# Kernel optimization log

Hardware: AMD Instinct MI355X
Metric: run time of the kernel (lower is better)

## Reference

```python
import jax, jax.numpy as jnp
import numpy as np

B, R, N, E, L = 2, 5, 1024, 3, 2
F_IN, D_DIFF = 64, 64
IN_RET, INTER, OUT_RET = 320, 256, 256
H1, H_RET, N_CLS = 128, 320, 2
GAMMA = 2.5


def _nrm(k, shape, s=0.05):
    return jax.random.normal(k, shape, jnp.float32) * s


def setup_inputs() -> dict:
    ks = jax.random.split(jax.random.key(0), 28)
    return {
        "x_batch": jax.random.normal(ks[0], (B, R, N, F_IN), jnp.float32),
        "a_batch": jax.random.uniform(ks[1], (B, R, N, N), jnp.float32),
        "T": _nrm(ks[2], (L, R, E, N, N), 0.02),
        "theta": _nrm(ks[3], (L, R, E), 0.1),
        "fc_w": _nrm(ks[4], (L, R, D_DIFF, D_DIFF)),
        "fc_b": _nrm(ks[5], (L, R, D_DIFF)),
        "conv_w": _nrm(ks[6], (L, R, R)),
        "conv_b": _nrm(ks[7], (L, R)),
        "a0": jnp.full((L,), 0.25, jnp.float32),
        "a1": jnp.full((L,), 0.25, jnp.float32),
        "qw": _nrm(ks[8], (L, INTER, IN_RET)),
        "qb": _nrm(ks[9], (L, INTER)),
        "kw": _nrm(ks[10], (L, INTER, IN_RET)),
        "kb": _nrm(ks[11], (L, INTER)),
        "vw": _nrm(ks[12], (L, INTER, IN_RET)),
        "vb": _nrm(ks[13], (L, INTER)),
        "rw": _nrm(ks[14], (L, OUT_RET, INTER)),
        "rb": _nrm(ks[15], (L, OUT_RET)),
        "a_ret": jnp.full((L,), 0.25, jnp.float32),
        "l1_w": _nrm(ks[16], (L, H1, H_RET)),
        "l1_b": _nrm(ks[17], (L, H1)),
        "l2_w": _nrm(ks[18], (L, H_RET, OUT_RET + H1)),
        "l2_b": _nrm(ks[19], (L, H_RET)),
        "mlp1_w": _nrm(ks[20], (H1, H_RET)),
        "mlp1_b": _nrm(ks[21], (H1,)),
        "mlp2_w": _nrm(ks[22], (N_CLS, H1)),
        "mlp2_b": _nrm(ks[23], (N_CLS,)),
        "a_mlp": jnp.asarray(0.25, jnp.float32),
    }


def _prelu(x, a):
    return jnp.where(x >= 0, x, a * x)


def reference(x_batch, a_batch, T, theta, fc_w, fc_b, conv_w, conv_b, a0, a1,
              qw, qb, kw, kb, vw, vb, rw, rb, a_ret,
              l1_w, l1_b, l2_w, l2_b, mlp1_w, mlp1_b, mlp2_w, mlp2_b, a_mlp):
    i = jnp.arange(N)
    # D_gamma buffer: torch code sets gamma**(-tril(ones,-1)) = 1/gamma on the strictly-lower triangle
    D_gamma = jnp.where(i[:, None] > i[None, :], 1.0 / GAMMA, 0.0).astype(x_batch.dtype)
    h = x_batch  # [B,R,N,F]
    skip = jnp.transpose(x_batch, (0, 2, 1, 3)).reshape(B, N, R * F_IN)  # layer-0 skip source [B,N,R*F]
    for l in range(L):
        # multi-relation diffusion: sum_e theta[r,e] * T[r,e] * A[b,r]
        S = jnp.einsum('re,renm->rnm', theta[l], T[l])          # [R,N,N]
        mats = S[None] * a_batch                                 # [B,R,N,N]
        feats = jnp.einsum('brnm,brmd->brnd', mats, h)           # [B,R,N,D]
        fc = jnp.einsum('brnd,rod->brno', feats, fc_w[l]) + fc_b[l][None, :, None, :]
        diff = _prelu(fc, a0[l])
        # 1x1 conv mixes the relation (channel) axis
        u = _prelu(jnp.einsum('sr,brno->bsno', conv_w[l], diff) + conv_b[l][None, :, None, None], a1[l])
        h = u
        # retention: view each [R,N,D] sample as (time_dim=N, in_dim=R*D) (raw row-major reshape)
        xr = u.reshape(B, N, IN_RET)
        q = xr @ qw[l].T + qb[l]
        k = xr @ kw[l].T + kb[l]
        v = xr @ vw[l].T + vb[l]
        scores = jnp.einsum('bti,bsi->bts', q, k)                # [B,N,N]
        ret = jnp.einsum('bts,bsi->bti', D_gamma[None] * scores, v)
        eta = _prelu(ret @ rw[l].T + rb[l], a_ret[l])            # [B,N,OUT_RET] (time_dim==N so view is identity)
        ts = skip @ l1_w[l].T + l1_b[l]                          # [B,N,H1]
        skip = jnp.concatenate([eta, ts], axis=2) @ l2_w[l].T + l2_b[l]  # [B,N,H_RET]
    out = _prelu(skip @ mlp1_w.T + mlp1_b, a_mlp)
    return out @ mlp2_w.T + mlp2_b                               # [B,N,N_CLS]
```

## Files before the change

### kernel.cpp

```cpp
#include <hip/hip_runtime.h>

#define NB 2
#define NR 5
#define NN_ 1024
#define NL 2
#define MSPLIT 4

__global__ void init_kernel(const float* __restrict__ x, float* __restrict__ skip) {
    int idx = blockIdx.x * 256 + threadIdx.x;
    int d4 = idx & 15;
    int n = (idx >> 4) & 1023;
    int br = idx >> 14;
    int b = br / NR, r = br % NR;
    float4 v = ((const float4*)x)[idx];
    *(float4*)(skip + ((size_t)b * NN_ + n) * 320 + r * 64 + d4 * 4) = v;
}

__global__ __launch_bounds__(256) void feats_kernel(
    const float* __restrict__ T, const float* __restrict__ theta,
    const float* __restrict__ a, const float* __restrict__ h,
    float* __restrict__ part, int l) {
    __shared__ float As[32][68];
    __shared__ float Ws[32][68];
    int br = blockIdx.y;
    int b = br / NR, r = br % NR;
    int n0 = blockIdx.x * 64;
    int mz = blockIdx.z;
    int tid = threadIdx.x;
    int tx = tid & 15, ty = tid >> 4;
    const float* Tb = T + (size_t)(l * NR + r) * 3145728;
    float th0 = theta[(l * NR + r) * 3 + 0];
    float th1 = theta[(l * NR + r) * 3 + 1];
    float th2 = theta[(l * NR + r) * 3 + 2];
    const float* ab = a + (size_t)(b * NR + r) * 1048576;
    const float* hb = h + (size_t)(b * NR + r) * 65536;
    int mbeg = mz * (NN_ / MSPLIT), mend = mbeg + NN_ / MSPLIT;
    int c4 = tid & 7, nrow = tid >> 3;
    int d4 = tid & 15, mrow = tid >> 4;
    float4 pT0[2], pT1[2], pT2[2], pA[2], pH[2];
    auto LOAD = [&](int k0) {
#pragma unroll
        for (int j = 0; j < 2; ++j) {
            size_t o = (size_t)(n0 + nrow + j * 32) * 1024 + k0 + c4 * 4;
            pT0[j] = *(const float4*)(Tb + o);
            pT1[j] = *(const float4*)(Tb + 1048576 + o);
            pT2[j] = *(const float4*)(Tb + 2097152 + o);
            pA[j]  = *(const float4*)(ab + o);
        }
#pragma unroll
        for (int j = 0; j < 2; ++j)
            pH[j] = *(const float4*)(hb + (size_t)(k0 + mrow + j * 16) * 64 + d4 * 4);
    };
    float acc[4][4] = {};
    LOAD(mbeg);
    for (int k0 = mbeg; k0 < mend; k0 += 32) {
        float4 w4[2];
#pragma unroll
        for (int j = 0; j < 2; ++j) {
            w4[j].x = (th0 * pT0[j].x + th1 * pT1[j].x + th2 * pT2[j].x) * pA[j].x;
            w4[j].y = (th0 * pT0[j].y + th1 * pT1[j].y + th2 * pT2[j].y) * pA[j].y;
            w4[j].z = (th0 * pT0[j].z + th1 * pT1[j].z + th2 * pT2[j].z) * pA[j].z;
            w4[j].w = (th0 * pT0[j].w + th1 * pT1[j].w + th2 * pT2[j].w) * pA[j].w;
        }
        __syncthreads();
#pragma unroll
        for (int j = 0; j < 2; ++j) {
            int n = nrow + j * 32;
            As[c4 * 4 + 0][n] = w4[j].x; As[c4 * 4 + 1][n] = w4[j].y;
            As[c4 * 4 + 2][n] = w4[j].z; As[c4 * 4 + 3][n] = w4[j].w;
        }
#pragma unroll
        for (int j = 0; j < 2; ++j)
            *(float4*)&Ws[mrow + j * 16][d4 * 4] = pH[j];
        if (k0 + 32 < mend) LOAD(k0 + 32);
        __syncthreads();
#pragma unroll
        for (int kk = 0; kk < 32; ++kk) {
            float4 ra = *(const float4*)&As[kk][ty * 4];
            float4 rw = *(const float4*)&Ws[kk][tx * 4];
            float ar[4] = {ra.x, ra.y, ra.z, ra.w};
            float wr[4] = {rw.x, rw.y, rw.z, rw.w};
#pragma unroll
            for (int i = 0; i < 4; ++i)
#pragma unroll
                for (int j = 0; j < 4; ++j) acc[i][j] += ar[i] * wr[j];
        }
    }
    float* pb = part + ((size_t)mz * 10 + br) * 65536;
#pragma unroll
    for (int i = 0; i < 4; ++i) {
        float4 o4 = make_float4(acc[i][0], acc[i][1], acc[i][2], acc[i][3]);
        *(float4*)(pb + (size_t)(n0 + ty * 4 + i) * 64 + tx * 4) = o4;
    }
}

__global__ __launch_bounds__(256) void reduce_fc_kernel(
    const float* __restrict__ part, const float* __restrict__ fc_w,
    const float* __restrict__ fc_b, const float* __restrict__ a0,
    float* __restrict__ diff, int l) {
    __shared__ float F[64][68];
    __shared__ float Wl[64][68];
    int br = blockIdx.y;
    int r = br % NR;
    int n0 = blockIdx.x * 64;
    int tid = threadIdx.x;
    int lane = tid & 63, g = tid >> 6;
#pragma unroll
    for (int j = 0; j < 4; ++j) {
        int d4 = g + j * 4;
        size_t off = (size_t)br * 65536 + (size_t)(n0 + lane) * 64 + d4 * 4;
        float4 s = *(const float4*)(part + off);
#pragma unroll
        for (int z = 1; z < MSPLIT; ++z) {
            float4 p = *(const float4*)(part + (size_t)z * 655360 + off);
            s.x += p.x; s.y += p.y; s.z += p.z; s.w += p.w;
        }
        F[d4 * 4 + 0][lane] = s.x; F[d4 * 4 + 1][lane] = s.y;
        F[d4 * 4 + 2][lane] = s.z; F[d4 * 4 + 3][lane] = s.w;
    }
    const float* w = fc_w + (size_t)(l * NR + r) * 4096;
#pragma unroll
    for (int j = 0; j < 4; ++j) {
        int d4 = g + j * 4;
        float4 wv = *(const float4*)(w + (size_t)lane * 64 + d4 * 4);
        Wl[d4 * 4 + 0][lane] = wv.x; Wl[d4 * 4 + 1][lane] = wv.y;
        Wl[d4 * 4 + 2][lane] = wv.z; Wl[d4 * 4 + 3][lane] = wv.w;
    }
    __syncthreads();
    int tx = tid & 15, ty = tid >> 4;
    float acc[4][4] = {};
#pragma unroll
    for (int kk = 0; kk < 64; ++kk) {
        float4 ra = *(const float4*)&F[kk][ty * 4];
        float4 rw = *(const float4*)&Wl[kk][tx * 4];
        float ar[4] = {ra.x, ra.y, ra.z, ra.w};
        float wr[4] = {rw.x, rw.y, rw.z, rw.w};
#pragma unroll
        for (int i = 0; i < 4; ++i)
#pragma unroll
            for (int j = 0; j < 4; ++j) acc[i][j] += ar[i] * wr[j];
    }
    float al = a0[l];
    const float* bia = fc_b + (l * NR + r) * 64;
#pragma unroll
    for (int i = 0; i < 4; ++i) {
        float4 o4;
        float* op = &o4.x;
#pragma unroll
        for (int j = 0; j < 4; ++j) {
            float v = acc[i][j] + bia[tx * 4 + j];
            op[j] = (v >= 0.f) ? v : al * v;
        }
        *(float4*)(diff + (size_t)br * 65536 + (size_t)(n0 + ty * 4 + i) * 64 + tx * 4) = o4;
    }
}

__global__ void conv_kernel(const float* __restrict__ diff,
                            const float* __restrict__ cw, const float* __restrict__ cb,
                            const float* __restrict__ a1, float* __restrict__ u, int l) {
    int idx = blockIdx.x * 256 + threadIdx.x;
    int no4 = idx & 16383;
    int bs = idx >> 14;
    int s = bs % NR, b = bs / NR;
    const float* dbase = diff + (size_t)b * NR * 65536;
    float bias = cb[l * NR + s];
    float4 acc = make_float4(bias, bias, bias, bias);
#pragma unroll
    for (int r = 0; r < NR; ++r) {
        float w = cw[(l * NR + s) * NR + r];
        float4 dv = *(const float4*)(dbase + (size_t)r * 65536 + no4 * 4);
        acc.x += w * dv.x; acc.y += w * dv.y; acc.z += w * dv.z; acc.w += w * dv.w;
    }
    float al = a1[l];
    acc.x = acc.x >= 0.f ? acc.x : al * acc.x;
    acc.y = acc.y >= 0.f ? acc.y : al * acc.y;
    acc.z = acc.z >= 0.f ? acc.z : al * acc.z;
    acc.w = acc.w >= 0.f ? acc.w : al * acc.w;
    *(float4*)(u + (size_t)bs * 65536 + no4 * 4) = acc;
}

struct BEnt {
    const float* A; const float* W; const float* bias; const float* alpha; float* C;
    int lda, K, Nw, ldc, w_nn, tri, trik;
};
struct BArg { BEnt e[4]; };

__global__ __launch_bounds__(256) void gemm_kernel(BArg bp) {
    BEnt E = bp.e[blockIdx.z];
    int m0 = blockIdx.y * 64, n0 = blockIdx.x * 64;
    if (n0 >= E.Nw) return;
    if (E.tri && (m0 + 63 <= n0)) return;
    int K = E.K;
    int kend = E.trik ? min(K, m0 + 64) : K;
    __shared__ float As[32][68];
    __shared__ float Ws[32][68];
    int tid = threadIdx.x;
    int c4 = tid & 7, row = tid >> 3;
    int n4 = tid & 15, krow = tid >> 4;
    int tx = tid & 15, ty = tid >> 4;
    const float* Ap = E.A; const float* Wp = E.W;
    int lda = E.lda, Nw = E.Nw;
    int wnn = E.w_nn;
    float4 pA[2], pW[2];
    auto LOAD = [&](int k0) {
#pragma unroll
        for (int j = 0; j < 2; ++j)
            pA[j] = *(const float4*)(Ap + (size_t)(m0 + row + j * 32) * lda + k0 + c4 * 4);
        if (!wnn) {
#pragma unroll
            for (int j = 0; j < 2; ++j)
                pW[j] = *(const float4*)(Wp + (size_t)(n0 + row + j * 32) * K + k0 + c4 * 4);
        } else {
#pragma unroll
            for (int j = 0; j < 2; ++j)
                pW[j] = *(const float4*)(Wp + (size_t)(k0 + krow + j * 16) * Nw + n0 + n4 * 4);
        }
    };
    float acc[4][4] = {};
    LOAD(0);
    for (int k0 = 0; k0 < kend; k0 += 32) {
        __syncthreads();
#pragma unroll
        for (int j = 0; j < 2; ++j) {
            int rr = row + j * 32;
            As[c4 * 4 + 0][rr] = pA[j].x; As[c4 * 4 + 1][rr] = pA[j].y;
            As[c4 * 4 + 2][rr] = pA[j].z; As[c4 * 4 + 3][rr] = pA[j].w;
        }
        if (!wnn) {
#pragma unroll
            for (int j = 0; j < 2; ++j) {
                int rr = row + j * 32;
                Ws[c4 * 4 + 0][rr] = pW[j].x; Ws[c4 * 4 + 1][rr] = pW[j].y;
                Ws[c4 * 4 + 2][rr] = pW[j].z; Ws[c4 * 4 + 3][rr] = pW[j].w;
            }
        } else {
#pragma unroll
            for (int j = 0; j < 2; ++j)
                *(float4*)&Ws[krow + j * 16][n4 * 4] = pW[j];
        }
        if (k0 + 32 < kend) LOAD(k0 + 32);
        __syncthreads();
#pragma unroll
        for (int kk = 0; kk < 32; ++kk) {
            float4 ra = *(const float4*)&As[kk][ty * 4];
            float4 rw = *(const float4*)&Ws[kk][tx * 4];
            float ar[4] = {ra.x, ra.y, ra.z, ra.w};
            float wr[4] = {rw.x, rw.y, rw.z, rw.w};
#pragma unroll
            for (int i = 0; i < 4; ++i)
#pragma unroll
                for (int j = 0; j < 4; ++j) acc[i][j] += ar[i] * wr[j];
        }
    }
    float al = E.alpha ? *E.alpha : 0.f;
#pragma unroll
    for (int i = 0; i < 4; ++i) {
        int m = m0 + ty * 4 + i;
        float4 o4;
        float* op = &o4.x;
#pragma unroll
        for (int j = 0; j < 4; ++j) {
            int n = n0 + tx * 4 + j;
            float v = acc[i][j];
            if (E.bias) v += E.bias[n];
            if (E.tri) v = (m > n) ? 0.4f * v : 0.f;
            if (E.alpha) v = (v >= 0.f) ? v : al * v;
            op[j] = v;
        }
        *(float4*)(E.C + (size_t)m * E.ldc + n0 + tx * 4) = o4;
    }
}

__global__ void final_kernel(const float* __restrict__ out1,
                             const float* __restrict__ w2, const float* __restrict__ b2,
                             float* __restrict__ out) {
    int idx = blockIdx.x * 256 + threadIdx.x;
    if (idx >= 2048 * 2) return;
    int m = idx >> 1, c = idx & 1;
    float acc = b2[c];
    const float* row = out1 + (size_t)m * 128;
#pragma unroll 8
    for (int dd = 0; dd < 128; ++dd) acc += row[dd] * w2[c * 128 + dd];
    out[idx] = acc;
}

extern "C" void kernel_launch(void* const* d_in, const int* in_sizes, int n_in,
                              void* d_out, int out_size, void* d_ws, size_t ws_size,
                              hipStream_t stream) {
    auto fp = [&](int i) { return (const float*)d_in[i]; };
    const float *x = fp(0), *a = fp(1), *T = fp(2), *theta = fp(3),
        *fc_w = fp(4), *fc_b = fp(5), *conv_w = fp(6), *conv_b = fp(7),
        *a0 = fp(8), *a1 = fp(9), *qw = fp(10), *qb = fp(11), *kw = fp(12), *kb = fp(13),
        *vw = fp(14), *vb = fp(15), *rw = fp(16), *rb = fp(17), *a_ret = fp(18),
        *l1_w = fp(19), *l1_b = fp(20), *l2_w = fp(21), *l2_b = fp(22),
        *m1w = fp(23), *m1b = fp(24), *m2w = fp(25), *m2b = fp(26), *a_mlp = fp(27);

    float* ws = (float*)d_ws;
    float* part = ws;   ws += MSPLIT * 655360;
    float* scores = part;
    float* u0 = ws;     ws += 655360;
    float* u1 = ws;     ws += 655360;
    float* skip = ws;   ws += 655360;
    float* diff = ws;   ws += 655360;
    float* q = ws;      ws += 524288;
    float* kk = ws;     ws += 524288;
    float* v = ws;      ws += 524288;
    float* ret = ws;    ws += 524288;
    float* cat = ws;    ws += 786432;
    float* out1 = ws;   ws += 262144;

    init_kernel<<<640, 256, 0, stream>>>(x, skip);
    for (int l = 0; l < NL; ++l) {
        const float* h = (l == 0) ? x : u0;
        float* u = (l == 0) ? u0 : u1;
        feats_kernel<<<dim3(16, 10, MSPLIT), 256, 0, stream>>>(T, theta, a, h, part, l);
        reduce_fc_kernel<<<dim3(16, 10), 256, 0, stream>>>(part, fc_w, fc_b, a0, diff, l);
        conv_kernel<<<640, 256, 0, stream>>>(diff, conv_w, conv_b, a1, u, l);
        {
            BArg g;
            g.e[0] = {u, qw + (size_t)l * 81920, qb + l * 256, nullptr, q, 320, 320, 256, 256, 0, 0, 0};
            g.e[1] = {u, kw + (size_t)l * 81920, kb + l * 256, nullptr, kk, 320, 320, 256, 256, 0, 0, 0};
            g.e[2] = {u, vw + (size_t)l * 81920, vb + l * 256, nullptr, v, 320, 320, 256, 256, 0, 0, 0};
            g.e[3] = {skip, l1_w + (size_t)l * 40960, l1_b + l * 128, nullptr, cat + 256, 320, 320, 128, 384, 0, 0, 0};
            gemm_kernel<<<dim3(4, 32, 4), 256, 0, stream>>>(g);
        }
        {
            BArg g;
            g.e[0] = {q, kk, nullptr, nullptr, scores, 256, 256, 1024, 1024, 0, 1, 0};
            g.e[1] = {q + 262144, kk + 262144, nullptr, nullptr, scores + 1048576, 256, 256, 1024, 1024, 0, 1, 0};
            g.e[2] = g.e[0]; g.e[3] = g.e[0];
            gemm_kernel<<<dim3(16, 16, 2), 256, 0, stream>>>(g);
        }
        {
            BArg g;
            g.e[0] = {scores, v, nullptr, nullptr, ret, 1024, 1024, 256, 256, 1, 0, 1};
            g.e[1] = {scores + 1048576, v + 262144, nullptr, nullptr, ret + 262144, 1024, 1024, 256, 256, 1, 0, 1};
            g.e[2] = g.e[0]; g.e[3] = g.e[0];
            gemm_kernel<<<dim3(4, 16, 2), 256, 0, stream>>>(g);
        }
        {
            BArg g;
            g.e[0] = {ret, rw + (size_t)l * 65536, rb + l * 256, a_ret + l, cat, 256, 256, 256, 384, 0, 0, 0};
            g.e[1] = g.e[0]; g.e[2] = g.e[0]; g.e[3] = g.e[0];
            gemm_kernel<<<dim3(4, 32, 1), 256, 0, stream>>>(g);
        }
        {
            BArg g;
            g.e[0] = {cat, l2_w + (size_t)l * 122880, l2_b + l * 320, nullptr, skip, 384, 384, 320, 320, 0, 0, 0};
            g.e[1] = g.e[0]; g.e[2] = g.e[0]; g.e[3] = g.e[0];
            gemm_kernel<<<dim3(5, 32, 1), 256, 0, stream>>>(g);
        }
    }
    {
        BArg g;
        g.e[0] = {skip, m1w, m1b, a_mlp, out1, 320, 320, 128, 128, 0, 0, 0};
        g.e[1] = g.e[0]; g.e[2] = g.e[0]; g.e[3] = g.e[0];
        gemm_kernel<<<dim3(2, 32, 1), 256, 0, stream>>>(g);
    }
    final_kernel<<<16, 256, 0, stream>>>(out1, m2w, m2b, (float*)d_out);
}
```

Measured before the change: 592.8 us.

## Double GEMM K-tile to 64 and split-K the retention scores×V GEMM

The shared GEMM kernel now stages 64-wide K tiles instead of 32, which halves the number of barrier-separated iterations but doubles shared memory to about 35 KB per block. The scores×V GEMM is split along K into two halves written to separate partial buffers, doubling its block count to fill more CUs. The two partials are summed while loading the A operand of the following ret×rw GEMM, so no extra reduction kernel is needed. Costs are lower occupancy from the larger LDS footprint, more registers for the prefetch buffers, and an extra partial buffer to read.

```diff
diff --git a/kernel.cpp b/kernel.cpp
--- a/kernel.cpp
+++ b/kernel.cpp
@@ -180,8 +180,9 @@
 }
 
 struct BEnt {
-    const float* A; const float* W; const float* bias; const float* alpha; float* C;
-    int lda, K, Nw, ldc, w_nn, tri, trik;
+    const float* A; const float* A2; const float* W; const float* bias;
+    const float* alpha; float* C;
+    int lda, Kcap, Nw, ldc, w_nn, tri, trik, kbeg;
 };
 struct BArg { BEnt e[4]; };
 
@@ -190,66 +191,72 @@
     int m0 = blockIdx.y * 64, n0 = blockIdx.x * 64;
     if (n0 >= E.Nw) return;
     if (E.tri && (m0 + 63 <= n0)) return;
-    int K = E.K;
-    int kend = E.trik ? min(K, m0 + 64) : K;
-    __shared__ float As[32][68];
-    __shared__ float Ws[32][68];
+    int kend = E.trik ? min(E.Kcap, m0 + 64) : E.Kcap;
+    __shared__ float As[64][68];
+    __shared__ float Ws[64][68];
     int tid = threadIdx.x;
-    int c4 = tid & 7, row = tid >> 3;
-    int n4 = tid & 15, krow = tid >> 4;
     int tx = tid & 15, ty = tid >> 4;
-    const float* Ap = E.A; const float* Wp = E.W;
-    int lda = E.lda, Nw = E.Nw;
-    int wnn = E.w_nn;
-    float4 pA[2], pW[2];
+    int ar = tid & 63, acg = tid >> 6;
+    int wr = tid >> 4, wc = tid & 15;
+    const float* Ap = E.A; const float* Ap2 = E.A2; const float* Wp = E.W;
+    int lda = E.lda, Kc = E.Kcap, Nw = E.Nw, wnn = E.w_nn;
+    float acc[4][4] = {};
+    float4 pA[4], pW[4];
     auto LOAD = [&](int k0) {
 #pragma unroll
-        for (int j = 0; j < 2; ++j)
-            pA[j] = *(const float4*)(Ap + (size_t)(m0 + row + j * 32) * lda + k0 + c4 * 4);
+        for (int j = 0; j < 4; ++j) {
+            size_t o = (size_t)(m0 + ar) * lda + k0 + (acg * 4 + j) * 4;
+            pA[j] = *(const float4*)(Ap + o);
+            if (Ap2) {
+                float4 t = *(const float4*)(Ap2 + o);
+                pA[j].x += t.x; pA[j].y += t.y; pA[j].z += t.z; pA[j].w += t.w;
+            }
+        }
         if (!wnn) {
 #pragma unroll
-            for (int j = 0; j < 2; ++j)
-                pW[j] = *(const float4*)(Wp + (size_t)(n0 + row + j * 32) * K + k0 + c4 * 4);
+            for (int j = 0; j < 4; ++j)
+                pW[j] = *(const float4*)(Wp + (size_t)(n0 + ar) * Kc + k0 + (acg * 4 + j) * 4);
         } else {
 #pragma unroll
-            for (int j = 0; j < 2; ++j)
-                pW[j] = *(const float4*)(Wp + (size_t)(k0 + krow + j * 16) * Nw + n0 + n4 * 4);
+            for (int j = 0; j < 4; ++j)
+                pW[j] = *(const float4*)(Wp + (size_t)(k0 + wr + j * 16) * Nw + n0 + wc * 4);
         }
     };
-    float acc[4][4] = {};
-    LOAD(0);
-    for (int k0 = 0; k0 < kend; k0 += 32) {
-        __syncthreads();
-#pragma unroll
-        for (int j = 0; j < 2; ++j) {
-            int rr = row + j * 32;
-            As[c4 * 4 + 0][rr] = pA[j].x; As[c4 * 4 + 1][rr] = pA[j].y;
-            As[c4 * 4 + 2][rr] = pA[j].z; As[c4 * 4 + 3][rr] = pA[j].w;
-        }
-        if (!wnn) {
-#pragma unroll
-            for (int j = 0; j < 2; ++j) {
-                int rr = row + j * 32;
-                Ws[c4 * 4 + 0][rr] = pW[j].x; Ws[c4 * 4 + 1][rr] = pW[j].y;
-                Ws[c4 * 4 + 2][rr] = pW[j].z; Ws[c4 * 4 + 3][rr] = pW[j].w;
+    if (E.kbeg < kend) {
+        LOAD(E.kbeg);
+        for (int k0 = E.kbeg; k0 < kend; k0 += 64) {
+            __syncthreads();
+#pragma unroll
+            for (int j = 0; j < 4; ++j) {
+                int kb = (acg * 4 + j) * 4;
+                As[kb + 0][ar] = pA[j].x; As[kb + 1][ar] = pA[j].y;
+                As[kb + 2][ar] = pA[j].z; As[kb + 3][ar] = pA[j].w;
             }
-        } else {
-#pragma unroll
-            for (int j = 0; j < 2; ++j)
-                *(float4*)&Ws[krow + j * 16][n4 * 4] = pW[j];
-        }
-        if (k0 + 32 < kend) LOAD(k0 + 32);
-        __syncthreads();
-#pragma unroll
-        for (int kk = 0; kk < 32; ++kk) {
-            float4 ra = *(const float4*)&As[kk][ty * 4];
-            float4 rw = *(const float4*)&Ws[kk][tx * 4];
-            float ar[4] = {ra.x, ra.y, ra.z, ra.w};
-            float wr[4] = {rw.x, rw.y, rw.z, rw.w};
-#pragma unroll
-            for (int i = 0; i < 4; ++i)
-#pragma unroll
-                for (int j = 0; j < 4; ++j) acc[i][j] += ar[i] * wr[j];
+            if (!wnn) {
+#pragma unroll
+                for (int j = 0; j < 4; ++j) {
+                    int kb = (acg * 4 + j) * 4;
+                    Ws[kb + 0][ar] = pW[j].x; Ws[kb + 1][ar] = pW[j].y;
+                    Ws[kb + 2][ar] = pW[j].z; Ws[kb + 3][ar] = pW[j].w;
+                }
+            } else {
+#pragma unroll
+                for (int j = 0; j < 4; ++j)
+                    *(float4*)&Ws[wr + j * 16][wc * 4] = pW[j];
+            }
+            if (k0 + 64 < kend) LOAD(k0 + 64);
+            __syncthreads();
+#pragma unroll
+            for (int kk = 0; kk < 64; ++kk) {
+                float4 ra = *(const float4*)&As[kk][ty * 4];
+                float4 rw = *(const float4*)&Ws[kk][tx * 4];
+                float arr[4] = {ra.x, ra.y, ra.z, ra.w};
+                float wrr[4] = {rw.x, rw.y, rw.z, rw.w};
+#pragma unroll
+                for (int i = 0; i < 4; ++i)
+#pragma unroll
+                    for (int j = 0; j < 4; ++j) acc[i][j] += arr[i] * wrr[j];
+            }
         }
     }
     float al = E.alpha ? *E.alpha : 0.f;
@@ -305,7 +312,8 @@
     float* q = ws;      ws += 524288;
     float* kk = ws;     ws += 524288;
     float* v = ws;      ws += 524288;
-    float* ret = ws;    ws += 524288;
+    float* retP0 = ws;  ws += 524288;
+    float* retP1 = ws;  ws += 524288;
     float* cat = ws;    ws += 786432;
     float* out1 = ws;   ws += 262144;
 
@@ -318,42 +326,44 @@
         conv_kernel<<<640, 256, 0, stream>>>(diff, conv_w, conv_b, a1, u, l);
         {
             BArg g;
-            g.e[0] = {u, qw + (size_t)l * 81920, qb + l * 256, nullptr, q, 320, 320, 256, 256, 0, 0, 0};
-            g.e[1] = {u, kw + (size_t)l * 81920, kb + l * 256, nullptr, kk, 320, 320, 256, 256, 0, 0, 0};
-            g.e[2] = {u, vw + (size_t)l * 81920, vb + l * 256, nullptr, v, 320, 320, 256, 256, 0, 0, 0};
-            g.e[3] = {skip, l1_w + (size_t)l * 40960, l1_b + l * 128, nullptr, cat + 256, 320, 320, 128, 384, 0, 0, 0};
+            g.e[0] = {u, nullptr, qw + (size_t)l * 81920, qb + l * 256, nullptr, q, 320, 320, 256, 256, 0, 0, 0, 0};
+            g.e[1] = {u, nullptr, kw + (size_t)l * 81920, kb + l * 256, nullptr, kk, 320, 320, 256, 256, 0, 0, 0, 0};
+            g.e[2] = {u, nullptr, vw + (size_t)l * 81920, vb + l * 256, nullptr, v, 320, 320, 256, 256, 0, 0, 0, 0};
+            g.e[3] = {skip, nullptr, l1_w + (size_t)l * 40960, l1_b + l * 128, nullptr, cat + 256, 320, 320, 128, 384, 0, 0, 0, 0};
             gemm_kernel<<<dim3(4, 32, 4), 256, 0, stream>>>(g);
         }
         {
             BArg g;
-            g.e[0] = {q, kk, nullptr, nullptr, scores, 256, 256, 1024, 1024, 0, 1, 0};
-            g.e[1] = {q + 262144, kk + 262144, nullptr, nullptr, scores + 1048576, 256, 256, 1024, 1024, 0, 1, 0};
+            g.e[0] = {q, nullptr, kk, nullptr, nullptr, scores, 256, 256, 1024, 1024, 0, 1, 0, 0};
+            g.e[1] = {q + 262144, nullptr, kk + 262144, nullptr, nullptr, scores + 1048576, 256, 256, 1024, 1024, 0, 1, 0, 0};
             g.e[2] = g.e[0]; g.e[3] = g.e[0];
             gemm_kernel<<<dim3(16, 16, 2), 256, 0, stream>>>(g);
         }
         {
             BArg g;
-            g.e[0] = {scores, v, nullptr, nullptr, ret, 1024, 1024, 256, 256, 1, 0, 1};
-            g.e[1] = {scores + 1048576, v + 262144, nullptr, nullptr, ret + 262144, 1024, 1024, 256, 256, 1, 0, 1};
-            g.e[2] = g.e[0]; g.e[3] = g.e[0];
-            gemm_kernel<<<dim3(4, 16, 2), 256, 0, stream>>>(g);
-        }
-        {
-            BArg g;
-            g.e[0] = {ret, rw + (size_t)l * 65536, rb + l * 256, a_ret + l, cat, 256, 256, 256, 384, 0, 0, 0};
+            for (int b = 0; b < 2; ++b)
+                for (int ks = 0; ks < 2; ++ks)
+                    g.e[b * 2 + ks] = {scores + (size_t)b * 1048576, nullptr, v + (size_t)b * 262144,
+                                       nullptr, nullptr, (ks ? retP1 : retP0) + (size_t)b * 262144,
+                                       1024, ks ? 1024 : 512, 256, 256, 1, 0, 1, ks ? 512 : 0};
+            gemm_kernel<<<dim3(4, 16, 4), 256, 0, stream>>>(g);
+        }
+        {
+            BArg g;
+            g.e[0] = {retP0, retP1, rw + (size_t)l * 65536, rb + l * 256, a_ret + l, cat, 256, 256, 256, 384, 0, 0, 0, 0};
             g.e[1] = g.e[0]; g.e[2] = g.e[0]; g.e[3] = g.e[0];
             gemm_kernel<<<dim3(4, 32, 1), 256, 0, stream>>>(g);
         }
         {
             BArg g;
-            g.e[0] = {cat, l2_w + (size_t)l * 122880, l2_b + l * 320, nullptr, skip, 384, 384, 320, 320, 0, 0, 0};
+            g.e[0] = {cat, nullptr, l2_w + (size_t)l * 122880, l2_b + l * 320, nullptr, skip, 384, 384, 320, 320, 0, 0, 0, 0};
             g.e[1] = g.e[0]; g.e[2] = g.e[0]; g.e[3] = g.e[0];
             gemm_kernel<<<dim3(5, 32, 1), 256, 0, stream>>>(g);
         }
     }
     {
         BArg g;
-        g.e[0] = {skip, m1w, m1b, a_mlp, out1, 320, 320, 128, 128, 0, 0, 0};
+        g.e[0] = {skip, nullptr, m1w, m1b, a_mlp, out1, 320, 320, 128, 128, 0, 0, 0, 0};
         g.e[1] = g.e[0]; g.e[2] = g.e[0]; g.e[3] = g.e[0];
         gemm_kernel<<<dim3(2, 32, 1), 256, 0, stream>>>(g);
     }
```

Result: slower. 610.0 us (+2.9%).
